# Kernel optimization log

Measured on AMD Instinct MI355X. Metric: run time of the kernel, lower is better.

## Reference

```python
import jax, jax.numpy as jnp
import numpy as np

N_NODES = 100000  # 2 node types x 50k
N_EDGES = 1600000


def setup_inputs() -> dict:
    key = jax.random.key(0)
    ks = jax.random.split(key, 16)
    feat0 = jax.random.normal(ks[0], (50000, 128), dtype=jnp.float32)
    feat1 = jax.random.normal(ks[1], (50000, 256), dtype=jnp.float32)
    edge_rows = jax.random.randint(ks[2], (N_EDGES,), 0, N_NODES, dtype=jnp.int32)
    edge_cols = jax.random.randint(ks[3], (N_EDGES,), 0, N_NODES, dtype=jnp.int32)
    edge_w = jax.random.uniform(ks[4], (N_EDGES,), dtype=jnp.float32)
    # fc_list: Linear(feat_dim, in_feat=128) per node type (torch Linear: x @ W.T + b)
    fc0_w = jax.random.normal(ks[5], (128, 128), dtype=jnp.float32) * 0.1
    fc0_b = jnp.zeros((128,), dtype=jnp.float32)
    fc1_w = jax.random.normal(ks[6], (128, 256), dtype=jnp.float32) * 0.07
    fc1_b = jnp.zeros((128,), dtype=jnp.float32)
    # GCNConv weights: W is [in, out] used as features @ W
    W1 = jax.random.normal(ks[7], (128, 128), dtype=jnp.float32) * 0.1  # in_feat -> 2*out_feat
    b1 = jnp.zeros((128,), dtype=jnp.float32)
    W2 = jax.random.normal(ks[8], (128, 64), dtype=jnp.float32) * 0.1   # 2*out_feat -> out_feat
    b2 = jnp.zeros((64,), dtype=jnp.float32)
    # predict: Linear(out_feat=64, num_class=8)
    pred_w = jax.random.normal(ks[9], (8, 64), dtype=jnp.float32) * 0.1
    pred_b = jnp.zeros((8,), dtype=jnp.float32)
    return {
        "feat0": feat0, "feat1": feat1,
        "fc0_w": fc0_w, "fc0_b": fc0_b, "fc1_w": fc1_w, "fc1_b": fc1_b,
        "W1": W1, "b1": b1, "W2": W2, "b2": b2,
        "pred_w": pred_w, "pred_b": pred_b,
        "edge_rows": edge_rows, "edge_cols": edge_cols, "edge_w": edge_w,
    }


def _spmm(edge_rows, edge_cols, edge_w, dense):
    # (sparse adj) @ dense : gather source rows, scale, scatter-add to dest rows
    msgs = dense[edge_cols] * edge_w[:, None]  # [E, F]
    return jax.ops.segment_sum(msgs, edge_rows, num_segments=N_NODES)


def reference(feat0, feat1, fc0_w, fc0_b, fc1_w, fc1_b, W1, b1, W2, b2,
              pred_w, pred_b, edge_rows, edge_cols, edge_w):
    # per-type projection (dropout is identity at p=0.0 / eval), then concat over nodes
    x0 = feat0 @ fc0_w.T + fc0_b
    x1 = feat1 @ fc1_w.T + fc1_b
    x = jnp.concatenate([x0, x1], axis=0)  # [N, 128]
    # GCN layer 1: relu(spmm(adj, x @ W1) + b1)
    x = jax.nn.relu(_spmm(edge_rows, edge_cols, edge_w, x @ W1) + b1)
    # GCN layer 2
    x = jax.nn.relu(_spmm(edge_rows, edge_cols, edge_w, x @ W2) + b2)
    # predict head
    return x @ pred_w.T + pred_b  # [N, num_class]
```

## Files before the change

kernel.cpp:

```cpp
#include <hip/hip_runtime.h>
#include <hip/hip_bf16.h>

#define N_NODES 100000
#define N_TYPE  50000
#define NB1     192
#define EPB1    8334
#define NBUCK2  196
#define CAP2    9216

typedef short bf16x8 __attribute__((ext_vector_type(8)));
typedef float f32x4  __attribute__((ext_vector_type(4)));
typedef unsigned short u16x4 __attribute__((ext_vector_type(4)));

__device__ inline unsigned short f2bf(float f) {
  union { float f; unsigned u; } x; x.f = f;
  unsigned r = (x.u + 0x7fff + ((x.u >> 16) & 1)) >> 16;
  return (unsigned short)r;
}
__device__ inline float bf2f(unsigned short h) {
  union { unsigned u; float f; } x; x.u = ((unsigned)h) << 16;
  return x.f;
}

__global__ __launch_bounds__(256) void prep_small_kernel(
    const float* __restrict__ fc0_w, const float* __restrict__ fc1_w,
    const float* __restrict__ fc0_b, const float* __restrict__ fc1_b,
    const float* __restrict__ W1, const float* __restrict__ W2,
    unsigned short* __restrict__ M0T, unsigned short* __restrict__ M1T,
    unsigned short* __restrict__ W2T, float* __restrict__ cb) {
  int idx = blockIdx.x * 256 + threadIdx.x;
  if (idx < 16384) {
    int i = idx >> 7, j = idx & 127;
    float s = 0.f;
    #pragma unroll 4
    for (int o = 0; o < 128; ++o) s = fmaf(fc0_w[o * 128 + i], W1[o * 128 + j], s);
    M0T[j * 128 + i] = f2bf(s);
  } else if (idx < 49152) {
    int r = idx - 16384;
    int i = r >> 7, j = r & 127;
    float s = 0.f;
    #pragma unroll 4
    for (int o = 0; o < 128; ++o) s = fmaf(fc1_w[o * 256 + i], W1[o * 128 + j], s);
    M1T[j * 256 + i] = f2bf(s);
  } else if (idx < 57344) {
    int r = idx - 49152;
    int k = r >> 6, n = r & 63;
    W2T[n * 128 + k] = f2bf(W2[k * 64 + n]);
  } else if (idx < 57600) {
    int r = idx - 57344;
    int t = r >> 7, j = r & 127;
    const float* bb = t ? fc1_b : fc0_b;
    float s = 0.f;
    for (int o = 0; o < 128; ++o) s = fmaf(bb[o], W1[o * 128 + j], s);
    cb[r] = s;
  }
}

template <int NC, int KTOT>
__global__ __launch_bounds__(256) void mfma_gemm_kernel(
    const float* __restrict__ A, const unsigned short* __restrict__ BT,
    const float* __restrict__ bc, unsigned short* __restrict__ Cout, int M) {
  constexpr int NREP = NC / 32;
  __shared__ unsigned short As[64 * 128];
  __shared__ unsigned short Bs[NC * 128];

  const int tid = threadIdx.x;
  const int row0 = blockIdx.x * 64;
  const int wave = tid >> 6, lane = tid & 63;
  const int wr = wave >> 1, wc = wave & 1;
  const int lm = lane & 15;
  const int lk16 = (lane >> 4) * 16;

  f32x4 acc[2][NREP];
  #pragma unroll
  for (int i = 0; i < 2; ++i)
    #pragma unroll
    for (int j = 0; j < NREP; ++j) acc[i][j] = (f32x4){0.f, 0.f, 0.f, 0.f};

  for (int kc = 0; kc < KTOT; kc += 128) {
    if (kc) __syncthreads();
    {
      const int r = tid >> 2;
      const int cg = tid & 3;
      int gr = row0 + r; if (gr > M - 1) gr = M - 1;
      const float* arow = A + (size_t)gr * KTOT + kc;
      char* asrow = (char*)As + r * 256;
      const int swz = (r & 7) << 4;
      #pragma unroll
      for (int i = 0; i < 8; ++i) {
        const int c = i * 4 + cg;
        float4 v = *(const float4*)(arow + c * 4);
        u16x4 q = {f2bf(v.x), f2bf(v.y), f2bf(v.z), f2bf(v.w)};
        *(u16x4*)(asrow + ((c * 8) ^ swz)) = q;
      }
    }
    {
      constexpr int CHUNKS = NC * 16;
      #pragma unroll
      for (int i = 0; i < CHUNKS / 256; ++i) {
        const int id = i * 256 + tid;
        const int n = id >> 4, k16 = id & 15;
        const uint4 w = *(const uint4*)((const char*)BT + ((size_t)n * KTOT + kc) * 2 + k16 * 16);
        *(uint4*)((char*)Bs + ((n * 256 + k16 * 16) ^ ((n & 7) << 4))) = w;
      }
    }
    __syncthreads();
    #pragma unroll
    for (int ks = 0; ks < 4; ++ks) {
      bf16x8 a[2];
      #pragma unroll
      for (int m = 0; m < 2; ++m) {
        const int r = wr * 32 + m * 16 + lm;
        a[m] = *(bf16x8*)((char*)As + ((r * 256 + ks * 64 + lk16) ^ ((r & 7) << 4)));
      }
      #pragma unroll
      for (int j = 0; j < NREP; ++j) {
        const int n = wc * (NC / 2) + j * 16 + lm;
        const bf16x8 b = *(bf16x8*)((char*)Bs + ((n * 256 + ks * 64 + lk16) ^ ((n & 7) << 4)));
        acc[0][j] = __builtin_amdgcn_mfma_f32_16x16x32_bf16(a[0], b, acc[0][j], 0, 0, 0);
        acc[1][j] = __builtin_amdgcn_mfma_f32_16x16x32_bf16(a[1], b, acc[1][j], 0, 0, 0);
      }
    }
  }
  #pragma unroll
  for (int m = 0; m < 2; ++m) {
    const int gr0 = row0 + wr * 32 + m * 16 + (lane >> 4) * 4;
    #pragma unroll
    for (int j = 0; j < NREP; ++j) {
      const int col = wc * (NC / 2) + j * 16 + lm;
      const float cbv = bc[col];
      #pragma unroll
      for (int i = 0; i < 4; ++i) {
        const int gr = gr0 + i;
        if (gr < M) Cout[(size_t)gr * NC + col] = f2bf(acc[m][j][i] + cbv);
      }
    }
  }
}

__global__ __launch_bounds__(256) void gemmA64_kernel(
    const unsigned short* __restrict__ A, const unsigned short* __restrict__ BT,
    unsigned short* __restrict__ Cout, int M) {
  __shared__ unsigned short As[64 * 128];
  __shared__ unsigned short Bs[64 * 128];
  const int tid = threadIdx.x;
  const int row0 = blockIdx.x * 64;
  const int wave = tid >> 6, lane = tid & 63;
  const int wr = wave >> 1, wc = wave & 1;
  const int lm = lane & 15, lk16 = (lane >> 4) * 16;
  {
    const int r = tid >> 2, cg = tid & 3;
    int gr = row0 + r; if (gr > M - 1) gr = M - 1;
    const uint4* arow = (const uint4*)(A + (size_t)gr * 128);
    const int swz = (r & 7) << 4;
    #pragma unroll
    for (int i = 0; i < 4; ++i) {
      const int c16 = i * 4 + cg;
      const uint4 w = arow[c16];
      *(uint4*)((char*)As + ((r * 256 + c16 * 16) ^ swz)) = w;
    }
  }
  #pragma unroll
  for (int i = 0; i < 4; ++i) {
    const int id = i * 256 + tid;
    const int n = id >> 4, k16 = id & 15;
    const uint4 w = *(const uint4*)((const char*)BT + n * 256 + k16 * 16);
    *(uint4*)((char*)Bs + ((n * 256 + k16 * 16) ^ ((n & 7) << 4))) = w;
  }
  __syncthreads();
  f32x4 acc[2][2];
  #pragma unroll
  for (int i = 0; i < 2; ++i)
    #pragma unroll
    for (int j = 0; j < 2; ++j) acc[i][j] = (f32x4){0.f, 0.f, 0.f, 0.f};
  #pragma unroll
  for (int ks = 0; ks < 4; ++ks) {
    bf16x8 a[2];
    #pragma unroll
    for (int m = 0; m < 2; ++m) {
      const int r = wr * 32 + m * 16 + lm;
      a[m] = *(bf16x8*)((char*)As + ((r * 256 + ks * 64 + lk16) ^ ((r & 7) << 4)));
    }
    #pragma unroll
    for (int j = 0; j < 2; ++j) {
      const int n = wc * 32 + j * 16 + lm;
      const bf16x8 b = *(bf16x8*)((char*)Bs + ((n * 256 + ks * 64 + lk16) ^ ((n & 7) << 4)));
      acc[0][j] = __builtin_amdgcn_mfma_f32_16x16x32_bf16(a[0], b, acc[0][j], 0, 0, 0);
      acc[1][j] = __builtin_amdgcn_mfma_f32_16x16x32_bf16(a[1], b, acc[1][j], 0, 0, 0);
    }
  }
  #pragma unroll
  for (int m = 0; m < 2; ++m) {
    const int gr0 = row0 + wr * 32 + m * 16 + (lane >> 4) * 4;
    #pragma unroll
    for (int j = 0; j < 2; ++j) {
      const int col = wc * 32 + j * 16 + lm;
      #pragma unroll
      for (int i = 0; i < 4; ++i) {
        const int gr = gr0 + i;
        if (gr < M) Cout[(size_t)gr * 64 + col] = f2bf(acc[m][j][i]);
      }
    }
  }
}

__global__ __launch_bounds__(512) void part1_kernel(
    const int* __restrict__ erow, const int* __restrict__ ecol,
    const float* __restrict__ ew, int* __restrict__ bcnt,
    uint2* __restrict__ tmp, int nE) {
  __shared__ int lh[256];
  __shared__ int lbase[256];
  __shared__ int srow[EPB1];
  const int t = threadIdx.x;
  const int e0 = blockIdx.x * EPB1;
  const int e1 = min(e0 + EPB1, nE);
  const int cnt = e1 - e0;
  for (int i = t; i < 256; i += 512) lh[i] = 0;
  __syncthreads();
  for (int i = t; i < cnt; i += 512) {
    const int r = erow[e0 + i];
    srow[i] = r;
    atomicAdd(&lh[r >> 9], 1);
  }
  __syncthreads();
  for (int i = t; i < NBUCK2; i += 512) {
    const int c = lh[i];
    lbase[i] = i * CAP2 + (c ? atomicAdd(&bcnt[i * 16], c) : 0);
  }
  __syncthreads();
  for (int i = t; i < 256; i += 512) lh[i] = 0;
  __syncthreads();
  for (int i = t; i < cnt; i += 512) {
    const int r = srow[i];
    const int b = r >> 9;
    const int pos = lbase[b] + atomicAdd(&lh[b], 1);
    const unsigned short bw = f2bf(ew[e0 + i]);
    const unsigned rec = ((unsigned)ecol[e0 + i] << 15) | (unsigned)bw;
    tmp[pos] = make_uint2(rec, (unsigned)r);
  }
}

__global__ __launch_bounds__(512) void part2_kernel(
    const int* __restrict__ bcnt, const uint2* __restrict__ tmp,
    unsigned* __restrict__ spack, int2* __restrict__ row_se, int N) {
  __shared__ int hist[512];
  __shared__ int scn[512];
  __shared__ int cur[512];
  const int b = blockIdx.x;
  const int r0 = b << 9;
  const int t = threadIdx.x;
  const int base = b * CAP2;
  const int cnt = bcnt[b * 16];
  const uint2* rec = tmp + base;
  hist[t] = 0;
  __syncthreads();
  for (int i = t; i < cnt; i += 512)
    atomicAdd(&hist[(int)rec[i].y - r0], 1);
  __syncthreads();
  const int v = hist[t];
  scn[t] = v;
  __syncthreads();
  #pragma unroll
  for (int off = 1; off < 512; off <<= 1) {
    int y = (t >= off) ? scn[t - off] : 0;
    __syncthreads();
    scn[t] += y;
    __syncthreads();
  }
  const int excl = base + scn[t] - v;
  const int r = r0 + t;
  if (r < N) row_se[r] = make_int2(excl, excl + v);
  cur[t] = excl;
  __syncthreads();
  for (int i = t; i < cnt; i += 512) {
    const uint2 rc = rec[i];
    const int pos = atomicAdd(&cur[(int)rc.y - r0], 1);
    spack[pos] = rc.x;
  }
}

__global__ __launch_bounds__(256) void spmm1_kernel(
    const unsigned short* __restrict__ h, const int2* __restrict__ row_se,
    const unsigned* __restrict__ spack, const float* __restrict__ b1,
    unsigned short* __restrict__ g1, int M) {
  const int r = (blockIdx.x * 256 + threadIdx.x) >> 5;
  const int lane = threadIdx.x & 31;
  if (r >= M) return;
  const int2 se = row_se[r];
  f32x4 acc = (f32x4){0.f, 0.f, 0.f, 0.f};
  int j = se.x;
  for (; j + 3 < se.y; j += 4) {
    const unsigned rc0 = spack[j], rc1 = spack[j + 1];
    const unsigned rc2 = spack[j + 2], rc3 = spack[j + 3];
    const u16x4 v0 = *(const u16x4*)(h + (size_t)(rc0 >> 15) * 128 + lane * 4);
    const u16x4 v1 = *(const u16x4*)(h + (size_t)(rc1 >> 15) * 128 + lane * 4);
    const u16x4 v2 = *(const u16x4*)(h + (size_t)(rc2 >> 15) * 128 + lane * 4);
    const u16x4 v3 = *(const u16x4*)(h + (size_t)(rc3 >> 15) * 128 + lane * 4);
    const float w0 = bf2f((unsigned short)(rc0 & 0x7fff));
    const float w1 = bf2f((unsigned short)(rc1 & 0x7fff));
    const float w2 = bf2f((unsigned short)(rc2 & 0x7fff));
    const float w3 = bf2f((unsigned short)(rc3 & 0x7fff));
    #pragma unroll
    for (int k = 0; k < 4; ++k) {
      acc[k] = fmaf(bf2f(v0[k]), w0, acc[k]);
      acc[k] = fmaf(bf2f(v1[k]), w1, acc[k]);
      acc[k] = fmaf(bf2f(v2[k]), w2, acc[k]);
      acc[k] = fmaf(bf2f(v3[k]), w3, acc[k]);
    }
  }
  for (; j < se.y; ++j) {
    const unsigned rc0 = spack[j];
    const u16x4 v0 = *(const u16x4*)(h + (size_t)(rc0 >> 15) * 128 + lane * 4);
    const float w0 = bf2f((unsigned short)(rc0 & 0x7fff));
    #pragma unroll
    for (int k = 0; k < 4; ++k) acc[k] = fmaf(bf2f(v0[k]), w0, acc[k]);
  }
  const float4 bb = *(const float4*)(b1 + lane * 4);
  u16x4 o;
  o[0] = f2bf(fmaxf(acc[0] + bb.x, 0.f));
  o[1] = f2bf(fmaxf(acc[1] + bb.y, 0.f));
  o[2] = f2bf(fmaxf(acc[2] + bb.z, 0.f));
  o[3] = f2bf(fmaxf(acc[3] + bb.w, 0.f));
  *(u16x4*)(g1 + (size_t)r * 128 + lane * 4) = o;
}

__global__ __launch_bounds__(256) void spmm2_kernel(
    const unsigned short* __restrict__ h2, const int2* __restrict__ row_se,
    const unsigned* __restrict__ spack, const float* __restrict__ pred_w,
    const float* __restrict__ b2, const float* __restrict__ pred_b,
    float* __restrict__ out, int M) {
  __shared__ float pw[512];
  __shared__ float bb2[64];
  __shared__ float pb[8];
  const int tid = threadIdx.x;
  for (int i = tid; i < 512; i += 256) pw[i] = pred_w[i];
  if (tid < 64) bb2[tid] = b2[tid];
  if (tid < 8) pb[tid] = pred_b[tid];
  __syncthreads();
  const int r = (blockIdx.x * 256 + tid) >> 5;
  const int lane = tid & 31;
  if (r >= M) return;
  const int2 se = row_se[r];
  float2 acc = make_float2(0.f, 0.f);
  int j = se.x;
  for (; j + 3 < se.y; j += 4) {
    const unsigned rc0 = spack[j], rc1 = spack[j + 1];
    const unsigned rc2 = spack[j + 2], rc3 = spack[j + 3];
    const ushort2 v0 = *(const ushort2*)(h2 + (size_t)(rc0 >> 15) * 64 + lane * 2);
    const ushort2 v1 = *(const ushort2*)(h2 + (size_t)(rc1 >> 15) * 64 + lane * 2);
    const ushort2 v2 = *(const ushort2*)(h2 + (size_t)(rc2 >> 15) * 64 + lane * 2);
    const ushort2 v3 = *(const ushort2*)(h2 + (size_t)(rc3 >> 15) * 64 + lane * 2);
    const float w0 = bf2f((unsigned short)(rc0 & 0x7fff));
    const float w1 = bf2f((unsigned short)(rc1 & 0x7fff));
    const float w2 = bf2f((unsigned short)(rc2 & 0x7fff));
    const float w3 = bf2f((unsigned short)(rc3 & 0x7fff));
    acc.x = fmaf(bf2f(v0.x), w0, acc.x);
    acc.y = fmaf(bf2f(v0.y), w0, acc.y);
    acc.x = fmaf(bf2f(v1.x), w1, acc.x);
    acc.y = fmaf(bf2f(v1.y), w1, acc.y);
    acc.x = fmaf(bf2f(v2.x), w2, acc.x);
    acc.y = fmaf(bf2f(v2.y), w2, acc.y);
    acc.x = fmaf(bf2f(v3.x), w3, acc.x);
    acc.y = fmaf(bf2f(v3.y), w3, acc.y);
  }
  for (; j < se.y; ++j) {
    const unsigned rc0 = spack[j];
    const ushort2 v0 = *(const ushort2*)(h2 + (size_t)(rc0 >> 15) * 64 + lane * 2);
    const float w0 = bf2f((unsigned short)(rc0 & 0x7fff));
    acc.x = fmaf(bf2f(v0.x), w0, acc.x);
    acc.y = fmaf(bf2f(v0.y), w0, acc.y);
  }
  const float a0 = fmaxf(acc.x + bb2[lane * 2], 0.f);
  const float a1 = fmaxf(acc.y + bb2[lane * 2 + 1], 0.f);
  float p[8];
  #pragma unroll
  for (int c = 0; c < 8; ++c)
    p[c] = a0 * pw[c * 64 + lane * 2] + a1 * pw[c * 64 + lane * 2 + 1];
  #pragma unroll
  for (int m = 1; m < 32; m <<= 1) {
    #pragma unroll
    for (int c = 0; c < 8; ++c) p[c] += __shfl_xor(p[c], m);
  }
  if (lane < 8) {
    float v = p[0];
    if (lane == 1) v = p[1];
    if (lane == 2) v = p[2];
    if (lane == 3) v = p[3];
    if (lane == 4) v = p[4];
    if (lane == 5) v = p[5];
    if (lane == 6) v = p[6];
    if (lane == 7) v = p[7];
    out[(size_t)r * 8 + lane] = v + pb[lane];
  }
}

__global__ void zero_kernel(float4* __restrict__ p, int n4) {
  int i = blockIdx.x * blockDim.x + threadIdx.x;
  const int stride = gridDim.x * blockDim.x;
  for (; i < n4; i += stride) p[i] = make_float4(0.f, 0.f, 0.f, 0.f);
}

extern "C" void kernel_launch(void* const* d_in, const int* in_sizes, int n_in,
                              void* d_out, int out_size, void* d_ws, size_t ws_size,
                              hipStream_t stream) {
  const float* feat0  = (const float*)d_in[0];
  const float* feat1  = (const float*)d_in[1];
  const float* fc0_w  = (const float*)d_in[2];
  const float* fc0_b  = (const float*)d_in[3];
  const float* fc1_w  = (const float*)d_in[4];
  const float* fc1_b  = (const float*)d_in[5];
  const float* W1     = (const float*)d_in[6];
  const float* b1     = (const float*)d_in[7];
  const float* W2     = (const float*)d_in[8];
  const float* b2     = (const float*)d_in[9];
  const float* pred_w = (const float*)d_in[10];
  const float* pred_b = (const float*)d_in[11];
  const int*   erow   = (const int*)d_in[12];
  const int*   ecol   = (const int*)d_in[13];
  const float* ew     = (const float*)d_in[14];
  float* out = (float*)d_out;
  const int nE = in_sizes[12];
  const int N = N_NODES;

  char* ws = (char*)d_ws;
  size_t off = 0;
  unsigned short* M0T = (unsigned short*)(ws + off); off += 32768;
  unsigned short* M1T = (unsigned short*)(ws + off); off += 65536;
  unsigned short* W2T = (unsigned short*)(ws + off); off += 16384;
  float* cb  = (float*)(ws + off); off += 1024;
  int* bcnt  = (int*)(ws + off); off += NBUCK2 * 64;
  uint2* tmp = (uint2*)(ws + off); off += (size_t)NBUCK2 * CAP2 * 8;
  unsigned* spack = (unsigned*)(ws + off); off += (size_t)NBUCK2 * CAP2 * 4;
  int2* row_se = (int2*)(ws + off); off += (size_t)N * 8;
  unsigned short* h  = (unsigned short*)(ws + off); off += (size_t)N * 128 * 2;
  unsigned short* g1 = (unsigned short*)(ws + off); off += (size_t)N * 128 * 2;
  unsigned short* h2 = (unsigned short*)(ws + off); off += (size_t)N * 64 * 2;

  hipLaunchKernelGGL(zero_kernel, dim3(4), dim3(256), 0, stream,
                     (float4*)bcnt, NBUCK2 * 64 / 16);
  hipLaunchKernelGGL(part1_kernel, dim3(NB1), dim3(512), 0, stream,
                     erow, ecol, ew, bcnt, tmp, nE);
  hipLaunchKernelGGL(part2_kernel, dim3(NBUCK2), dim3(512), 0, stream,
                     bcnt, tmp, spack, row_se, N);

  hipLaunchKernelGGL(prep_small_kernel, dim3(225), dim3(256), 0, stream,
                     fc0_w, fc1_w, fc0_b, fc1_b, W1, W2, M0T, M1T, W2T, cb);
  hipLaunchKernelGGL((mfma_gemm_kernel<128, 128>), dim3((N_TYPE + 63) / 64), dim3(256),
                     0, stream, feat0, M0T, cb, h, N_TYPE);
  hipLaunchKernelGGL((mfma_gemm_kernel<128, 256>), dim3((N_TYPE + 63) / 64), dim3(256),
                     0, stream, feat1, M1T, cb + 128, h + (size_t)N_TYPE * 128, N_TYPE);
  hipLaunchKernelGGL(spmm1_kernel, dim3((N * 32 + 255) / 256), dim3(256), 0, stream,
                     h, row_se, spack, b1, g1, N);
  hipLaunchKernelGGL(gemmA64_kernel, dim3((N + 63) / 64), dim3(256), 0, stream,
                     g1, W2T, h2, N);
  hipLaunchKernelGGL(spmm2_kernel, dim3((N * 32 + 255) / 256), dim3(256), 0, stream,
                     h2, row_se, spack, pred_w, b2, pred_b, out, N);
}
```

Before: 222.0 us.

## Split edge bucketing into histogram/scan/scatter and move predict head to MFMA kernel

The edge partition pass is replaced by three kernels: a per-block bucket histogram, a single-block scan that computes deterministic per-block bucket offsets, and a scatter. This removes the global atomics and the large shared row buffer. Separately, the predict head is taken out of spmm2, which no longer does the per-row shuffle reduction over 8 classes. spmm2 now writes a bf16 intermediate g2, and a new MFMA head kernel multiplies it by a padded bf16 copy of pred_w. The cost is an extra read of erow, a serial single-block scan, an extra g2 round trip through memory, and lower precision for pred_w.

```diff
diff --git a/kernel.cpp b/kernel.cpp
--- a/kernel.cpp
+++ b/kernel.cpp
@@ -26,8 +26,10 @@
     const float* __restrict__ fc0_w, const float* __restrict__ fc1_w,
     const float* __restrict__ fc0_b, const float* __restrict__ fc1_b,
     const float* __restrict__ W1, const float* __restrict__ W2,
+    const float* __restrict__ pred_w,
     unsigned short* __restrict__ M0T, unsigned short* __restrict__ M1T,
-    unsigned short* __restrict__ W2T, float* __restrict__ cb) {
+    unsigned short* __restrict__ W2T, unsigned short* __restrict__ pwT,
+    float* __restrict__ cb) {
   int idx = blockIdx.x * 256 + threadIdx.x;
   if (idx < 16384) {
     int i = idx >> 7, j = idx & 127;
@@ -53,6 +55,10 @@
     float s = 0.f;
     for (int o = 0; o < 128; ++o) s = fmaf(bb[o], W1[o * 128 + j], s);
     cb[r] = s;
+  } else if (idx < 58624) {
+    int r = idx - 57600;
+    int n = r >> 6, k = r & 63;
+    pwT[r] = (n < 8) ? f2bf(pred_w[n * 64 + k]) : (unsigned short)0;
   }
 }
 
@@ -204,38 +210,51 @@
   }
 }
 
-__global__ __launch_bounds__(512) void part1_kernel(
+__global__ __launch_bounds__(512) void hist1_kernel(
+    const int* __restrict__ erow, int* __restrict__ gh, int nE) {
+  __shared__ int lh[256];
+  const int t = threadIdx.x;
+  const int e0 = blockIdx.x * EPB1;
+  const int e1 = min(e0 + EPB1, nE);
+  for (int i = t; i < 256; i += 512) lh[i] = 0;
+  __syncthreads();
+  for (int i = e0 + t; i < e1; i += 512) atomicAdd(&lh[erow[i] >> 9], 1);
+  __syncthreads();
+  for (int i = t; i < NBUCK2; i += 512) gh[i * NB1 + blockIdx.x] = lh[i];
+}
+
+__global__ __launch_bounds__(256) void scan_kernel(
+    const int* __restrict__ gh, int* __restrict__ gbase, int* __restrict__ bcnt) {
+  const int t = threadIdx.x;
+  if (t >= NBUCK2) return;
+  int run = t * CAP2;
+  for (int blk = 0; blk < NB1; ++blk) {
+    gbase[blk * 256 + t] = run;
+    run += gh[t * NB1 + blk];
+  }
+  bcnt[t] = run - t * CAP2;
+}
+
+__global__ __launch_bounds__(512) void scatter1_kernel(
     const int* __restrict__ erow, const int* __restrict__ ecol,
-    const float* __restrict__ ew, int* __restrict__ bcnt,
+    const float* __restrict__ ew, const int* __restrict__ gbase,
     uint2* __restrict__ tmp, int nE) {
   __shared__ int lh[256];
   __shared__ int lbase[256];
-  __shared__ int srow[EPB1];
   const int t = threadIdx.x;
   const int e0 = blockIdx.x * EPB1;
   const int e1 = min(e0 + EPB1, nE);
-  const int cnt = e1 - e0;
-  for (int i = t; i < 256; i += 512) lh[i] = 0;
-  __syncthreads();
-  for (int i = t; i < cnt; i += 512) {
-    const int r = erow[e0 + i];
-    srow[i] = r;
-    atomicAdd(&lh[r >> 9], 1);
-  }
-  __syncthreads();
-  for (int i = t; i < NBUCK2; i += 512) {
-    const int c = lh[i];
-    lbase[i] = i * CAP2 + (c ? atomicAdd(&bcnt[i * 16], c) : 0);
-  }
-  __syncthreads();
-  for (int i = t; i < 256; i += 512) lh[i] = 0;
-  __syncthreads();
-  for (int i = t; i < cnt; i += 512) {
-    const int r = srow[i];
+  for (int i = t; i < 256; i += 512) {
+    lh[i] = 0;
+    lbase[i] = (i < NBUCK2) ? gbase[blockIdx.x * 256 + i] : 0;
+  }
+  __syncthreads();
+  for (int i = e0 + t; i < e1; i += 512) {
+    const int r = erow[i];
     const int b = r >> 9;
     const int pos = lbase[b] + atomicAdd(&lh[b], 1);
-    const unsigned short bw = f2bf(ew[e0 + i]);
-    const unsigned rec = ((unsigned)ecol[e0 + i] << 15) | (unsigned)bw;
+    const unsigned short bw = f2bf(ew[i]);
+    const unsigned rec = ((unsigned)ecol[i] << 15) | (unsigned)bw;
     tmp[pos] = make_uint2(rec, (unsigned)r);
   }
 }
@@ -250,7 +269,7 @@
   const int r0 = b << 9;
   const int t = threadIdx.x;
   const int base = b * CAP2;
-  const int cnt = bcnt[b * 16];
+  const int cnt = bcnt[b];
   const uint2* rec = tmp + base;
   hist[t] = 0;
   __syncthreads();
@@ -326,19 +345,10 @@
 
 __global__ __launch_bounds__(256) void spmm2_kernel(
     const unsigned short* __restrict__ h2, const int2* __restrict__ row_se,
-    const unsigned* __restrict__ spack, const float* __restrict__ pred_w,
-    const float* __restrict__ b2, const float* __restrict__ pred_b,
-    float* __restrict__ out, int M) {
-  __shared__ float pw[512];
-  __shared__ float bb2[64];
-  __shared__ float pb[8];
-  const int tid = threadIdx.x;
-  for (int i = tid; i < 512; i += 256) pw[i] = pred_w[i];
-  if (tid < 64) bb2[tid] = b2[tid];
-  if (tid < 8) pb[tid] = pred_b[tid];
-  __syncthreads();
-  const int r = (blockIdx.x * 256 + tid) >> 5;
-  const int lane = tid & 31;
+    const unsigned* __restrict__ spack, const float* __restrict__ b2,
+    unsigned short* __restrict__ g2, int M) {
+  const int r = (blockIdx.x * 256 + threadIdx.x) >> 5;
+  const int lane = threadIdx.x & 31;
   if (r >= M) return;
   const int2 se = row_se[r];
   float2 acc = make_float2(0.f, 0.f);
@@ -370,34 +380,54 @@
     acc.x = fmaf(bf2f(v0.x), w0, acc.x);
     acc.y = fmaf(bf2f(v0.y), w0, acc.y);
   }
-  const float a0 = fmaxf(acc.x + bb2[lane * 2], 0.f);
-  const float a1 = fmaxf(acc.y + bb2[lane * 2 + 1], 0.f);
-  float p[8];
-  #pragma unroll
-  for (int c = 0; c < 8; ++c)
-    p[c] = a0 * pw[c * 64 + lane * 2] + a1 * pw[c * 64 + lane * 2 + 1];
-  #pragma unroll
-  for (int m = 1; m < 32; m <<= 1) {
-    #pragma unroll
-    for (int c = 0; c < 8; ++c) p[c] += __shfl_xor(p[c], m);
-  }
-  if (lane < 8) {
-    float v = p[0];
-    if (lane == 1) v = p[1];
-    if (lane == 2) v = p[2];
-    if (lane == 3) v = p[3];
-    if (lane == 4) v = p[4];
-    if (lane == 5) v = p[5];
-    if (lane == 6) v = p[6];
-    if (lane == 7) v = p[7];
-    out[(size_t)r * 8 + lane] = v + pb[lane];
-  }
-}
-
-__global__ void zero_kernel(float4* __restrict__ p, int n4) {
-  int i = blockIdx.x * blockDim.x + threadIdx.x;
-  const int stride = gridDim.x * blockDim.x;
-  for (; i < n4; i += stride) p[i] = make_float4(0.f, 0.f, 0.f, 0.f);
+  const float a0 = fmaxf(acc.x + b2[lane * 2], 0.f);
+  const float a1 = fmaxf(acc.y + b2[lane * 2 + 1], 0.f);
+  ushort2 o;
+  o.x = f2bf(a0);
+  o.y = f2bf(a1);
+  *(ushort2*)(g2 + (size_t)r * 64 + lane * 2) = o;
+}
+
+__global__ __launch_bounds__(256) void head_kernel(
+    const unsigned short* __restrict__ g2, const unsigned short* __restrict__ pwT,
+    const float* __restrict__ pred_b, float* __restrict__ out, int M) {
+  __shared__ unsigned short As[64 * 64];
+  __shared__ unsigned short Bs[16 * 64];
+  const int tid = threadIdx.x;
+  const int wave = tid >> 6, lane = tid & 63;
+  const int row0 = blockIdx.x * 64;
+  if (tid < 128) {
+    const int n = tid >> 3, k16 = tid & 7;
+    const uint4 w = *(const uint4*)((const char*)pwT + n * 128 + k16 * 16);
+    *(uint4*)((char*)Bs + ((n * 128 + k16 * 16) ^ ((n & 7) << 4))) = w;
+  }
+  #pragma unroll
+  for (int i = 0; i < 2; ++i) {
+    const int id = i * 256 + tid;
+    const int rr = id >> 3, k16 = id & 7;
+    int gr = row0 + rr; if (gr > M - 1) gr = M - 1;
+    const uint4 w = *(const uint4*)(g2 + (size_t)gr * 64 + k16 * 8);
+    *(uint4*)((char*)As + ((rr * 128 + k16 * 16) ^ ((rr & 7) << 4))) = w;
+  }
+  __syncthreads();
+  const int lm = lane & 15, lk16 = (lane >> 4) * 16;
+  f32x4 acc4 = (f32x4){0.f, 0.f, 0.f, 0.f};
+  #pragma unroll
+  for (int ks = 0; ks < 2; ++ks) {
+    const int rrow = wave * 16 + lm;
+    const bf16x8 a = *(bf16x8*)((char*)As + ((rrow * 128 + ks * 64 + lk16) ^ ((rrow & 7) << 4)));
+    const bf16x8 b = *(bf16x8*)((char*)Bs + ((lm * 128 + ks * 64 + lk16) ^ ((lm & 7) << 4)));
+    acc4 = __builtin_amdgcn_mfma_f32_16x16x32_bf16(a, b, acc4, 0, 0, 0);
+  }
+  if (lm < 8) {
+    const float pbv = pred_b[lm];
+    const int gr0 = row0 + wave * 16 + (lane >> 4) * 4;
+    #pragma unroll
+    for (int i = 0; i < 4; ++i) {
+      const int gr = gr0 + i;
+      if (gr < M) out[(size_t)gr * 8 + lm] = acc4[i] + pbv;
+    }
+  }
 }
 
 extern "C" void kernel_launch(void* const* d_in, const int* in_sizes, int n_in,
@@ -427,24 +457,29 @@
   unsigned short* M0T = (unsigned short*)(ws + off); off += 32768;
   unsigned short* M1T = (unsigned short*)(ws + off); off += 65536;
   unsigned short* W2T = (unsigned short*)(ws + off); off += 16384;
-  float* cb  = (float*)(ws + off); off += 1024;
-  int* bcnt  = (int*)(ws + off); off += NBUCK2 * 64;
-  uint2* tmp = (uint2*)(ws + off); off += (size_t)NBUCK2 * CAP2 * 8;
+  unsigned short* pwT = (unsigned short*)(ws + off); off += 2048;
+  float* cb   = (float*)(ws + off); off += 1024;
+  int* gh     = (int*)(ws + off); off += (size_t)NBUCK2 * NB1 * 4;
+  int* gbase  = (int*)(ws + off); off += (size_t)NB1 * 256 * 4;
+  int* bcnt   = (int*)(ws + off); off += 1024;
+  uint2* tmp  = (uint2*)(ws + off); off += (size_t)NBUCK2 * CAP2 * 8;
   unsigned* spack = (unsigned*)(ws + off); off += (size_t)NBUCK2 * CAP2 * 4;
   int2* row_se = (int2*)(ws + off); off += (size_t)N * 8;
   unsigned short* h  = (unsigned short*)(ws + off); off += (size_t)N * 128 * 2;
   unsigned short* g1 = (unsigned short*)(ws + off); off += (size_t)N * 128 * 2;
   unsigned short* h2 = (unsigned short*)(ws + off); off += (size_t)N * 64 * 2;
-
-  hipLaunchKernelGGL(zero_kernel, dim3(4), dim3(256), 0, stream,
-                     (float4*)bcnt, NBUCK2 * 64 / 16);
-  hipLaunchKernelGGL(part1_kernel, dim3(NB1), dim3(512), 0, stream,
-                     erow, ecol, ew, bcnt, tmp, nE);
+  unsigned short* g2 = (unsigned short*)(ws + off); off += (size_t)N * 64 * 2;
+
+  hipLaunchKernelGGL(hist1_kernel, dim3(NB1), dim3(512), 0, stream, erow, gh, nE);
+  hipLaunchKernelGGL(scan_kernel, dim3(1), dim3(256), 0, stream, gh, gbase, bcnt);
+  hipLaunchKernelGGL(scatter1_kernel, dim3(NB1), dim3(512), 0, stream,
+                     erow, ecol, ew, gbase, tmp, nE);
   hipLaunchKernelGGL(part2_kernel, dim3(NBUCK2), dim3(512), 0, stream,
                      bcnt, tmp, spack, row_se, N);
 
-  hipLaunchKernelGGL(prep_small_kernel, dim3(225), dim3(256), 0, stream,
-                     fc0_w, fc1_w, fc0_b, fc1_b, W1, W2, M0T, M1T, W2T, cb);
+  hipLaunchKernelGGL(prep_small_kernel, dim3(229), dim3(256), 0, stream,
+                     fc0_w, fc1_w, fc0_b, fc1_b, W1, W2, pred_w,
+                     M0T, M1T, W2T, pwT, cb);
   hipLaunchKernelGGL((mfma_gemm_kernel<128, 128>), dim3((N_TYPE + 63) / 64), dim3(256),
                      0, stream, feat0, M0T, cb, h, N_TYPE);
   hipLaunchKernelGGL((mfma_gemm_kernel<128, 256>), dim3((N_TYPE + 63) / 64), dim3(256),
@@ -454,5 +489,7 @@
   hipLaunchKernelGGL(gemmA64_kernel, dim3((N + 63) / 64), dim3(256), 0, stream,
                      g1, W2T, h2, N);
   hipLaunchKernelGGL(spmm2_kernel, dim3((N * 32 + 255) / 256), dim3(256), 0, stream,
-                     h2, row_se, spack, pred_w, b2, pred_b, out, N);
-}
+                     h2, row_se, spack, b2, g2, N);
+  hipLaunchKernelGGL(head_kernel, dim3((N + 63) / 64), dim3(256), 0, stream,
+                     g2, pwT, pred_b, out, N);
+}
```

New measurement: 209.5 us. 1.06x faster.
